# Optimization experiments

Measured on AMD Instinct MI355X. Metric: run time of the kernel, lower is better.

## Reference

```python
import jax, jax.numpy as jnp
import numpy as np

N, CF, CC, H, W, S = 16, 768, 64, 56, 56, 40  # S = feature_samples
EPS = 1e-10


def _norm(t):
    # F.normalize(t, dim=1, eps=1e-10): divide by channel L2 norm clamped to eps
    n = jnp.sqrt(jnp.sum(t * t, axis=1, keepdims=True))
    return t / jnp.maximum(n, EPS)


def _grid_sample(t, grid):
    """Bilinear grid_sample, padding_mode='border', align_corners=True.
    t: [N,C,H,W]; grid: [N,Ho,Wo,2] with (x,y) in [-1,1]. Returns [N,C,Ho,Wo]."""
    Ht, Wt = t.shape[2], t.shape[3]
    x = (grid[..., 0] + 1.0) * 0.5 * (Wt - 1)
    y = (grid[..., 1] + 1.0) * 0.5 * (Ht - 1)
    # border padding == clamp sampling coords to valid range
    x = jnp.clip(x, 0.0, Wt - 1)
    y = jnp.clip(y, 0.0, Ht - 1)
    x0 = jnp.floor(x)
    y0 = jnp.floor(y)
    wx = (x - x0)[:, None]  # [N,1,Ho,Wo]
    wy = (y - y0)[:, None]
    x0i = x0.astype(jnp.int32)
    y0i = y0.astype(jnp.int32)
    x1i = jnp.minimum(x0i + 1, Wt - 1)
    y1i = jnp.minimum(y0i + 1, Ht - 1)

    def gather(img, yi, xi):  # img [C,H,W], yi/xi [Ho,Wo] -> [C,Ho,Wo]
        return img[:, yi, xi]

    g = jax.vmap(gather)
    v00 = g(t, y0i, x0i)
    v01 = g(t, y0i, x1i)
    v10 = g(t, y1i, x0i)
    v11 = g(t, y1i, x1i)
    return (v00 * (1 - wx) * (1 - wy) + v01 * wx * (1 - wy)
            + v10 * (1 - wx) * wy + v11 * wx * wy)


def _corr(a, b):
    return jnp.einsum('nchw,ncij->nhwij', a, b)


def setup_inputs() -> dict:
    key = jax.random.key(0)
    k = jax.random.split(key, 6)
    return {
        'orig_feats': jax.random.normal(k[0], (N, CF, H, W), jnp.float32),
        'orig_feats_pos': jax.random.normal(k[1], (N, CF, H, W), jnp.float32),
        'orig_code': jax.random.normal(k[2], (N, CC, H, W), jnp.float32),
        'orig_code_pos': jax.random.normal(k[3], (N, CC, H, W), jnp.float32),
        'coords1': jax.random.uniform(k[4], (N, S, S, 2), jnp.float32),
        'coords2': jax.random.uniform(k[5], (N, S, S, 2), jnp.float32),
    }


def reference(orig_feats, orig_feats_pos, orig_code, orig_code_pos, coords1, coords2):
    # torch.rand(...)*2 - 1, then sample() permutes grid dims (0,2,1,3)
    g1 = jnp.transpose(coords1 * 2.0 - 1.0, (0, 2, 1, 3))
    g2 = jnp.transpose(coords2 * 2.0 - 1.0, (0, 2, 1, 3))
    feats = _grid_sample(orig_feats, g1)
    code = _grid_sample(orig_code, g1)
    feats_pos = _grid_sample(orig_feats_pos, g2)
    code_pos = _grid_sample(orig_code_pos, g2)

    fd = _corr(_norm(feats), _norm(feats_pos))           # [N,S,S,S,S]
    old_mean = jnp.mean(fd)
    fd = fd - jnp.mean(fd, axis=(3, 4), keepdims=True)
    fd = fd - jnp.mean(fd) + old_mean
    cd = _corr(_norm(code), _norm(code_pos))             # [N,S,S,S,S]
    loss = jnp.mean(-jnp.maximum(cd, 0.0) * fd)
    return loss
```

## Files before the change

### kernel.cpp

```cpp
#include <hip/hip_runtime.h>
#include <hip/hip_bf16.h>

#define NN 16
#define CF 768
#define CC 64
#define HH 56
#define WW 56
#define SS 40
#define PP (SS*SS)
#define PPAD 1664
#define NPT (NN*PP)
#define NPTP (NN*PPAD)
#define HWP (HH*WW)

typedef __attribute__((ext_vector_type(8))) short short8;
typedef __attribute__((ext_vector_type(4))) float f32x4;

typedef const __attribute__((address_space(1))) void* gas_p;
typedef __attribute__((address_space(3))) void* las_p;

__device__ __forceinline__ unsigned f2b(float f) {
    __hip_bfloat16 b = __float2bfloat16(f);
    return (unsigned)*(unsigned short*)&b;
}
__device__ __forceinline__ float bup(unsigned u, int hi) {
    unsigned bits = hi ? (u & 0xffff0000u) : (u << 16);
    return __uint_as_float(bits);
}

__device__ __forceinline__ void bilin(float gx, float gy,
    int& o00, int& o01, int& o10, int& o11,
    float& w00, float& w01, float& w10, float& w11)
{
    float x = (gx + 1.f) * 0.5f * (float)(WW - 1);
    float y = (gy + 1.f) * 0.5f * (float)(HH - 1);
    x = fminf(fmaxf(x, 0.f), (float)(WW - 1));
    y = fminf(fmaxf(y, 0.f), (float)(HH - 1));
    float xf = floorf(x), yf = floorf(y);
    int x0 = (int)xf, y0 = (int)yf;
    int x1 = min(x0 + 1, WW - 1), y1 = min(y0 + 1, HH - 1);
    float wx = x - xf, wy = y - yf;
    w00 = (1.f-wx)*(1.f-wy); w01 = wx*(1.f-wy); w10 = (1.f-wx)*wy; w11 = wx*wy;
    o00 = y0*WW + x0; o01 = y0*WW + x1; o10 = y1*WW + x0; o11 = y1*WW + x1;
}

__global__ __launch_bounds__(256) void k_sample(
    const float* __restrict__ f0, const float* __restrict__ f1,
    const float* __restrict__ c0in, const float* __restrict__ c1in,
    const float* __restrict__ g0, const float* __restrict__ g1,
    float* __restrict__ nrmF, float* __restrict__ nrmC,
    unsigned char* __restrict__ OF0, unsigned char* __restrict__ OF1,
    short* __restrict__ OC0, short* __restrict__ OC1)
{
    const int flat = blockIdx.x;
    const int q    = (flat >> 3) & 3;
    const int u    = ((flat >> 5) << 3) | (flat & 7);
    const int set  = u / 416;
    const int rem  = u % 416;
    const int n    = rem / 26;
    const int v    = rem % 26;
    const bool isF = v < 24;
    const int ks   = isF ? v : v - 24;
    const int g    = ks * 4 + q;

    const float* src0; float* nrm;
    if (isF) {
        src0 = (set ? f1 : f0) + ((size_t)n * CF + g * 8) * HWP;
        nrm  = nrmF + (size_t)set * NPTP;
    } else {
        src0 = (set ? c1in : c0in) + ((size_t)n * CC + g * 8) * HWP;
        nrm  = nrmC + (size_t)set * NPTP;
    }
    unsigned char* outF = set ? OF1 : OF0;
    short*         outC = set ? OC1 : OC0;
    const float* gr = set ? g1 : g0;
    const int t = threadIdx.x;

    __shared__ float plane[2][4096];

    int   po[7], pdx[7], pdw[7];
    float pw[7][4];
    #pragma unroll
    for (int i = 0; i < 7; i++) {
        int p = t + i * 256;
        if (p < PP) {
            float2 gg = *(const float2*)&gr[2 * (n * PP + p)];
            int o00, o01, o10, o11; float w00, w01, w10, w11;
            bilin(gg.x*2.f - 1.f, gg.y*2.f - 1.f, o00, o01, o10, o11, w00, w01, w10, w11);
            po[i] = o00; pdx[i] = o01 - o00; pdw[i] = o10 - o00;
            pw[i][0] = w00; pw[i][1] = w01; pw[i][2] = w10; pw[i][3] = w11;
        } else {
            po[i] = 0; pdx[i] = 0; pdw[i] = 0;
            pw[i][0] = pw[i][1] = pw[i][2] = pw[i][3] = 0.f;
        }
    }

    auto* pl3 = (__attribute__((address_space(3))) char*)&plane[0][0];

#define ISSUE(C)                                                                    \
    do {                                                                            \
        const char* sp_ = (const char*)(src0 + (C) * HWP);                          \
        _Pragma("unroll")                                                           \
        for (int i_ = 0; i_ < 4; i_++) {                                            \
            int j_  = t + i_ * 256;                                                 \
            int jc_ = min(j_, 783);                                                 \
            __builtin_amdgcn_global_load_lds((gas_p)(sp_ + jc_ * 16),               \
                (las_p)(pl3 + (((C) & 1) * 16384 + j_ * 16)), 16, 0, 0);            \
        }                                                                           \
    } while (0)

    float ss[7];
    float fv[7][8];
    #pragma unroll
    for (int i = 0; i < 7; i++) ss[i] = 0.f;

    ISSUE(0);
    #pragma unroll
    for (int c = 0; c < 8; c++) {
        if (c < 7) {
            ISSUE(c + 1);
            asm volatile("s_waitcnt vmcnt(4)" ::: "memory");
        } else {
            asm volatile("s_waitcnt vmcnt(0)" ::: "memory");
        }
        __builtin_amdgcn_sched_barrier(0);
        __builtin_amdgcn_s_barrier();
        const float* pl = &plane[c & 1][0];
        #pragma unroll
        for (int i = 0; i < 7; i++) {
            float val = pw[i][0] * pl[po[i]]
                      + pw[i][1] * pl[po[i] + pdx[i]]
                      + pw[i][2] * pl[po[i] + pdw[i]]
                      + pw[i][3] * pl[po[i] + pdw[i] + pdx[i]];
            ss[i] += val * val;
            fv[i][c] = val;
        }
        __builtin_amdgcn_sched_barrier(0);
        __builtin_amdgcn_s_barrier();
    }
#undef ISSUE

    if (isF) {
        const size_t ob = ((size_t)((n * 24 + ks) * 4 + q)) * PPAD * 8;
        #pragma unroll
        for (int i = 0; i < 7; i++) {
            int p = t + i * 256;
            if (p < PPAD) {
                unsigned w0 = 0u, w1 = 0u;
                w0 = __builtin_amdgcn_cvt_pk_fp8_f32(fv[i][0], fv[i][1], w0, 0);
                w0 = __builtin_amdgcn_cvt_pk_fp8_f32(fv[i][2], fv[i][3], w0, 1);
                w1 = __builtin_amdgcn_cvt_pk_fp8_f32(fv[i][4], fv[i][5], w1, 0);
                w1 = __builtin_amdgcn_cvt_pk_fp8_f32(fv[i][6], fv[i][7], w1, 1);
                uint2 w; w.x = w0; w.y = w1;
                *(uint2*)&outF[ob + (size_t)p * 8] = w;
                if (p < PP) atomicAdd(&nrm[n * PPAD + p], ss[i]);
            }
        }
    } else {
        const size_t ob = ((size_t)(n * 2 + ks)) * PPAD * 32 + q * 8;
        #pragma unroll
        for (int i = 0; i < 7; i++) {
            int p = t + i * 256;
            if (p < PPAD) {
                short ov[8] __attribute__((aligned(16)));
                #pragma unroll
                for (int c = 0; c < 8; c++) {
                    __hip_bfloat16 b = __float2bfloat16(fv[i][c]);
                    ov[c] = *(short*)&b;
                }
                *(short8*)&outC[ob + (size_t)p * 32] = *(const short8*)ov;
                if (p < PP) atomicAdd(&nrm[n * PPAD + p], ss[i]);
            }
        }
    }
}

__global__ __launch_bounds__(256) void k_nrm(
    const float* __restrict__ nrmF, const float* __restrict__ nrmC,
    float* __restrict__ sclF, float* __restrict__ sclC)
{
    const int i = blockIdx.x * 256 + threadIdx.x;
    if (i >= 2 * NPTP) return;
    const float* nrm = blockIdx.y ? nrmC : nrmF;
    float*       scl = blockIdx.y ? sclC : sclF;
    const int p = i % PPAD;
    float s = (p < PP) ? 1.f / fmaxf(sqrtf(nrm[i]), 1e-10f) : 0.f;
    scl[i] = s;
}

__global__ __launch_bounds__(256, 3) void k_corr(
    const unsigned char* __restrict__ A, const unsigned char* __restrict__ B,
    const short* __restrict__ C, const short* __restrict__ D,
    const float* __restrict__ sF, const float* __restrict__ sC,
    float* __restrict__ rowfd, float* __restrict__ rowrc, float* __restrict__ t1out)
{
    const int flat = blockIdx.x;
    const int v   = (flat & 7) * 338 + (flat >> 3);
    const int n   = v / 169;
    const int rr  = v - n * 169;
    const int bp1 = (rr / 13) * 128;
    const int bp2 = (rr % 13) * 128;

    __shared__ char Asb[3][8192];
    __shared__ char Bsb[3][8192];

    const int t    = threadIdx.x;
    const int wv   = t >> 6, lane = t & 63;
    const int wm   = wv >> 1, wn = wv & 1;
    const int frow = lane & 15, fcg = lane >> 4;
    const int fslot = fcg ^ ((frow >> 1) & 3);

    const int sg0  = wv * 2 * 64 + lane;
    const int row0 = sg0 >> 2,        cg0 = (sg0 & 3) ^ ((row0 >> 1) & 3);
    const int sg1  = sg0 + 64;
    const int row1 = sg1 >> 2,        cg1 = (sg1 & 3) ^ ((row1 >> 1) & 3);
    const size_t kstep_s = (size_t)PPAD * 32;
    const short* cdC = C + (size_t)n * 2 * kstep_s;
    const short* cdD = D + (size_t)n * 2 * kstep_s;
    const size_t toA0 = (size_t)(bp1 + row0) * 32 + cg0 * 8;
    const size_t toA1 = (size_t)(bp1 + row1) * 32 + cg1 * 8;
    const size_t toB0 = (size_t)(bp2 + row0) * 32 + cg0 * 8;
    const size_t toB1 = (size_t)(bp2 + row1) * 32 + cg1 * 8;
    auto* As3s = (__attribute__((address_space(3))) short*)&Asb[0][0];
    auto* Bs3s = (__attribute__((address_space(3))) short*)&Bsb[0][0];
    const short* AsS = (const short*)&Asb[0][0];
    const short* BsS = (const short*)&Bsb[0][0];
    const int ldsA0 = (wv * 2    ) * 512;
    const int ldsA1 = (wv * 2 + 1) * 512;

    const size_t FDTILE = (size_t)PPAD * 64;
    const unsigned char* fdA = A + (size_t)n * 24 * ((size_t)PPAD * 32);
    const unsigned char* fdB = B + (size_t)n * 24 * ((size_t)PPAD * 32);
    const size_t toAf0 = (size_t)(wv * 2    ) * (PPAD * 8) + (size_t)(bp1 + 2 * lane) * 8;
    const size_t toAf1 = (size_t)(wv * 2 + 1) * (PPAD * 8) + (size_t)(bp1 + 2 * lane) * 8;
    const size_t toBf0 = (size_t)(wv * 2    ) * (PPAD * 8) + (size_t)(bp2 + 2 * lane) * 8;
    const size_t toBf1 = (size_t)(wv * 2 + 1) * (PPAD * 8) + (size_t)(bp2 + 2 * lane) * 8;
    auto* Asb3 = (__attribute__((address_space(3))) char*)&Asb[0][0];
    auto* Bsb3 = (__attribute__((address_space(3))) char*)&Bsb[0][0];
    const int fldsW0 = (wv * 2    ) * 1024;
    const int fldsW1 = (wv * 2 + 1) * 1024;

#define STAGECD(BUF, OFF)                                                           \
    do {                                                                            \
        const size_t off_ = (OFF);                                                  \
        const int b_ = (BUF) * 4096;                                                \
        __builtin_amdgcn_global_load_lds((gas_p)(cdC + toA0 + off_),                \
                                         (las_p)(As3s + b_ + ldsA0), 16, 0, 0);     \
        __builtin_amdgcn_global_load_lds((gas_p)(cdC + toA1 + off_),                \
                                         (las_p)(As3s + b_ + ldsA1), 16, 0, 0);     \
        __builtin_amdgcn_global_load_lds((gas_p)(cdD + toB0 + off_),                \
                                         (las_p)(Bs3s + b_ + ldsA0), 16, 0, 0);     \
        __builtin_amdgcn_global_load_lds((gas_p)(cdD + toB1 + off_),                \
                                         (las_p)(Bs3s + b_ + ldsA1), 16, 0, 0);     \
    } while (0)

#define STAGEF(TILE, BUF)                                                           \
    do {                                                                            \
        const size_t off_ = (size_t)(TILE) * FDTILE;                                \
        __builtin_amdgcn_global_load_lds((gas_p)(fdA + toAf0 + off_),               \
                                         (las_p)(Asb3 + (BUF) * 8192 + fldsW0), 16, 0, 0); \
        __builtin_amdgcn_global_load_lds((gas_p)(fdA + toAf1 + off_),               \
                                         (las_p)(Asb3 + (BUF) * 8192 + fldsW1), 16, 0, 0); \
        __builtin_amdgcn_global_load_lds((gas_p)(fdB + toBf0 + off_),               \
                                         (las_p)(Bsb3 + (BUF) * 8192 + fldsW0), 16, 0, 0); \
        __builtin_amdgcn_global_load_lds((gas_p)(fdB + toBf1 + off_),               \
                                         (las_p)(Bsb3 + (BUF) * 8192 + fldsW1), 16, 0, 0); \
    } while (0)

#define COMPUTECD(BUF, ACC)                                                         \
    do {                                                                            \
        short8 af[4], bf[4];                                                        \
        _Pragma("unroll")                                                           \
        for (int m = 0; m < 4; m++)                                                 \
            af[m] = *(const short8*)&AsS[(BUF)*4096 + (wm*64 + m*16 + frow)*32 + fslot*8]; \
        _Pragma("unroll")                                                           \
        for (int q = 0; q < 4; q++)                                                 \
            bf[q] = *(const short8*)&BsS[(BUF)*4096 + (wn*64 + q*16 + frow)*32 + fslot*8]; \
        _Pragma("unroll")                                                           \
        for (int m = 0; m < 4; m++)                                                 \
            _Pragma("unroll")                                                       \
            for (int q = 0; q < 4; q++)                                             \
                ACC[m][q] = __builtin_amdgcn_mfma_f32_16x16x32_bf16(af[m], bf[q], ACC[m][q], 0, 0, 0); \
    } while (0)

#define COMPUTEF64(BUF, ACC)                                                        \
    do {                                                                            \
        _Pragma("unroll")                                                           \
        for (int kk_ = 0; kk_ < 2; kk_++) {                                         \
            long af[4], bf[4];                                                      \
            const int kb_ = (BUF) * 8192 + (kk_ * 4 + fcg) * 1024;                  \
            _Pragma("unroll")                                                       \
            for (int m = 0; m < 4; m++)                                             \
                af[m] = *(const long*)&Asb[0][kb_ + (wm*64 + m*16 + frow)*8];       \
            _Pragma("unroll")                                                       \
            for (int q = 0; q < 4; q++)                                             \
                bf[q] = *(const long*)&Bsb[0][kb_ + (wn*64 + q*16 + frow)*8];       \
            _Pragma("unroll")                                                       \
            for (int m = 0; m < 4; m++)                                             \
                _Pragma("unroll")                                                   \
                for (int q = 0; q < 4; q++)                                         \
                    ACC[m][q] = __builtin_amdgcn_mfma_f32_16x16x32_fp8_fp8(af[m], bf[q], ACC[m][q], 0, 0, 0); \
        }                                                                           \
    } while (0)

#define WAITV4  do { asm volatile("s_waitcnt vmcnt(4)" ::: "memory");               \
                     __builtin_amdgcn_sched_barrier(0);                             \
                     __builtin_amdgcn_s_barrier(); } while (0)
#define WAITV0  do { asm volatile("s_waitcnt vmcnt(0)" ::: "memory");               \
                     __builtin_amdgcn_sched_barrier(0);                             \
                     __builtin_amdgcn_s_barrier(); } while (0)

    unsigned pcd[4][4][2];

    STAGECD(0, 0);
    STAGECD(1, kstep_s);

    {
        f32x4 acccd[4][4];
        #pragma unroll
        for (int m = 0; m < 4; m++)
            #pragma unroll
            for (int q = 0; q < 4; q++)
                #pragma unroll
                for (int r = 0; r < 4; r++) acccd[m][q][r] = 0.f;

        WAITV4;
        STAGEF(0, 2);
        COMPUTECD(0, acccd);
        WAITV4;
        STAGEF(1, 0);
        COMPUTECD(1, acccd);

        #pragma unroll
        for (int m = 0; m < 4; m++)
            #pragma unroll
            for (int q = 0; q < 4; q++) {
                float r0 = fmaxf(acccd[m][q][0], 0.f);
                float r1 = fmaxf(acccd[m][q][1], 0.f);
                float r2 = fmaxf(acccd[m][q][2], 0.f);
                float r3 = fmaxf(acccd[m][q][3], 0.f);
                pcd[m][q][0] = f2b(r0) | (f2b(r1) << 16);
                pcd[m][q][1] = f2b(r2) | (f2b(r3) << 16);
            }
    }

    f32x4 accfd[4][4];
    #pragma unroll
    for (int m = 0; m < 4; m++)
        #pragma unroll
        for (int q = 0; q < 4; q++)
            #pragma unroll
            for (int r = 0; r < 4; r++) accfd[m][q][r] = 0.f;

    for (int kp = 0; kp < 4; kp++) {
        const int tb = 3 * kp;
        WAITV4;
        STAGEF(tb + 2, 1);
        COMPUTEF64(2, accfd);
        WAITV4;
        if (kp < 3) STAGEF(tb + 3, 2);
        COMPUTEF64(0, accfd);
        if (kp < 3) {
            WAITV4;
            STAGEF(tb + 4, 0);
        } else {
            WAITV0;
        }
        COMPUTEF64(1, accfd);
    }
#undef STAGECD
#undef STAGEF
#undef COMPUTECD
#undef COMPUTEF64
#undef WAITV4
#undef WAITV0

    float scc_[4], sfc_[4];
    #pragma unroll
    for (int q = 0; q < 4; q++) {
        size_t colp = (size_t)NPTP + (size_t)n * PPAD + bp2 + wn*64 + q*16 + frow;
        scc_[q] = sC[colp];
        sfc_[q] = sF[colp];
    }

    float t1 = 0.f;
    #pragma unroll
    for (int m = 0; m < 4; m++) {
        #pragma unroll
        for (int r = 0; r < 4; r++) {
            size_t rowp = (size_t)n * PPAD + bp1 + wm*64 + m*16 + fcg*4 + r;
            float scr = sC[rowp];
            float sfr = sF[rowp];
            float sf = 0.f, sr = 0.f;
            #pragma unroll
            for (int q = 0; q < 4; q++) {
                float fdv = accfd[m][q][r] * sfr * sfc_[q];
                float rcv = bup(pcd[m][q][r >> 1], r & 1) * scr * scc_[q];
                t1 += rcv * fdv;
                sf += fdv;
                sr += rcv;
            }
            #pragma unroll
            for (int d = 1; d < 16; d <<= 1) {
                sf += __shfl_xor(sf, d, 64);
                sr += __shfl_xor(sr, d, 64);
            }
            if ((lane & 15) == 0) {
                int row = bp1 + wm*64 + m*16 + fcg*4 + r;
                atomicAdd(&rowfd[n * PPAD + row], sf);
                atomicAdd(&rowrc[n * PPAD + row], sr);
            }
        }
    }
    #pragma unroll
    for (int d = 1; d < 64; d <<= 1) t1 += __shfl_xor(t1, d, 64);
    __shared__ float t1s[4];
    if (lane == 0) t1s[wv] = t1;
    __syncthreads();
    if (t == 0) atomicAdd(t1out, t1s[0] + t1s[1] + t1s[2] + t1s[3]);
}

__global__ __launch_bounds__(1024) void k_final(
    const float* __restrict__ rowfd, const float* __restrict__ rowrc,
    const float* __restrict__ t1p, float* __restrict__ out)
{
    const int t = threadIdx.x;
    double cr = 0.0, sf = 0.0, sr = 0.0;
    for (int i = t; i < NN * PPAD; i += 1024) {
        double a = rowfd[i], b = rowrc[i];
        cr += a * b; sf += a; sr += b;
    }
    __shared__ double sh[1024];
    sh[t] = cr; __syncthreads();
    for (int s = 512; s > 0; s >>= 1) { if (t < s) sh[t] += sh[t + s]; __syncthreads(); }
    cr = sh[0]; __syncthreads();
    sh[t] = sf; __syncthreads();
    for (int s = 512; s > 0; s >>= 1) { if (t < s) sh[t] += sh[t + s]; __syncthreads(); }
    sf = sh[0]; __syncthreads();
    sh[t] = sr; __syncthreads();
    for (int s = 512; s > 0; s >>= 1) { if (t < s) sh[t] += sh[t + s]; __syncthreads(); }
    sr = sh[0];
    if (t == 0) {
        double M = (double)NN * (double)PP * (double)PP;
        double t1 = (double)t1p[0];
        double bracket = t1 - cr / (double)PP + (sf / M) * sr;
        out[0] = (float)(-bracket / M);
    }
}

extern "C" void kernel_launch(void* const* d_in, const int* in_sizes, int n_in,
                              void* d_out, int out_size, void* d_ws, size_t ws_size,
                              hipStream_t stream)
{
    const float* orig_feats     = (const float*)d_in[0];
    const float* orig_feats_pos = (const float*)d_in[1];
    const float* orig_code      = (const float*)d_in[2];
    const float* orig_code_pos  = (const float*)d_in[3];
    const float* coords1        = (const float*)d_in[4];
    const float* coords2        = (const float*)d_in[5];

    char* ws = (char*)d_ws;
    float* t1    = (float*)(ws + 0);
    float* rowfd = (float*)(ws + 256);
    float* rowrc = (float*)(ws + 106752);
    float* nrmF  = (float*)(ws + 213248);
    float* nrmC  = (float*)(ws + 426240);
    const size_t zeroBytes = 639232;
    float* sclF  = (float*)(ws + 639232);
    float* sclC  = (float*)(ws + 852224);
    unsigned char* OF0 = (unsigned char*)(ws + 1065216);
    unsigned char* OF1 = (unsigned char*)(ws + 1065216 + 20447232ull);
    short* OC0 = (short*)(ws + 1065216 + 2*20447232ull);
    short* OC1 = (short*)(ws + 1065216 + 2*20447232ull + 3407872ull);

    (void)hipMemsetAsync(d_ws, 0, zeroBytes, stream);

    k_sample<<<dim3(3328), 256, 0, stream>>>(
        orig_feats, orig_feats_pos, orig_code, orig_code_pos,
        coords1, coords2, nrmF, nrmC, OF0, OF1, OC0, OC1);

    k_nrm<<<dim3((2*NPTP + 255)/256, 2), 256, 0, stream>>>(
        nrmF, nrmC, sclF, sclC);

    k_corr<<<dim3(2704), 256, 0, stream>>>(
        OF0, OF1, OC0, OC1, sclF, sclC, rowfd, rowrc, t1);

    k_final<<<1, 1024, 0, stream>>>(rowfd, rowrc, t1, (float*)d_out);
}
```

Measured before the change: 211.5 us.

## Widen correlation tile to 128x256 with 512 threads and compute code correlation at epilogue

The correlation kernel now uses 512-thread blocks with 8 waves, each block covering a 128x256 output tile. This halves the block count and raises reuse of the A-side feature data. The code-correlation MFMAs move from a prologue, where results were packed to bf16 to save registers, to an epilogue that recomputes them per row group from data staged after the feature loop. That removes the bf16 rounding of the code correlation and frees registers held across the main loop. The cost is a larger LDS footprint, clamped padded columns in the last tile column that do wasted work, and an extra serial staging phase before the epilogue.

```diff
diff --git a/kernel.cpp b/kernel.cpp
--- a/kernel.cpp
+++ b/kernel.cpp
@@ -18,15 +18,6 @@
 
 typedef const __attribute__((address_space(1))) void* gas_p;
 typedef __attribute__((address_space(3))) void* las_p;
-
-__device__ __forceinline__ unsigned f2b(float f) {
-    __hip_bfloat16 b = __float2bfloat16(f);
-    return (unsigned)*(unsigned short*)&b;
-}
-__device__ __forceinline__ float bup(unsigned u, int hi) {
-    unsigned bits = hi ? (u & 0xffff0000u) : (u << 16);
-    return __uint_as_float(bits);
-}
 
 __device__ __forceinline__ void bilin(float gx, float gy,
     int& o00, int& o01, int& o10, int& o11,
@@ -188,110 +179,93 @@
     scl[i] = s;
 }
 
-__global__ __launch_bounds__(256, 3) void k_corr(
+__global__ __launch_bounds__(512, 4) void k_corr(
     const unsigned char* __restrict__ A, const unsigned char* __restrict__ B,
     const short* __restrict__ C, const short* __restrict__ D,
     const float* __restrict__ sF, const float* __restrict__ sC,
     float* __restrict__ rowfd, float* __restrict__ rowrc, float* __restrict__ t1out)
 {
     const int flat = blockIdx.x;
-    const int v   = (flat & 7) * 338 + (flat >> 3);
-    const int n   = v / 169;
-    const int rr  = v - n * 169;
-    const int bp1 = (rr / 13) * 128;
-    const int bp2 = (rr % 13) * 128;
+    const int v   = (flat & 7) * 182 + (flat >> 3);
+    const int n   = v / 91;
+    const int rr  = v - n * 91;
+    const int bp1 = (rr / 7) * 128;
+    const int bp2 = (rr % 7) * 256;
 
     __shared__ char Asb[3][8192];
-    __shared__ char Bsb[3][8192];
+    __shared__ char Bsb[3][16384];
+    __shared__ float t1s[8];
 
     const int t    = threadIdx.x;
     const int wv   = t >> 6, lane = t & 63;
-    const int wm   = wv >> 1, wn = wv & 1;
+    const int wm   = wv >> 2, wn = wv & 3;
     const int frow = lane & 15, fcg = lane >> 4;
     const int fslot = fcg ^ ((frow >> 1) & 3);
-
-    const int sg0  = wv * 2 * 64 + lane;
-    const int row0 = sg0 >> 2,        cg0 = (sg0 & 3) ^ ((row0 >> 1) & 3);
-    const int sg1  = sg0 + 64;
-    const int row1 = sg1 >> 2,        cg1 = (sg1 & 3) ^ ((row1 >> 1) & 3);
-    const size_t kstep_s = (size_t)PPAD * 32;
-    const short* cdC = C + (size_t)n * 2 * kstep_s;
-    const short* cdD = D + (size_t)n * 2 * kstep_s;
-    const size_t toA0 = (size_t)(bp1 + row0) * 32 + cg0 * 8;
-    const size_t toA1 = (size_t)(bp1 + row1) * 32 + cg1 * 8;
-    const size_t toB0 = (size_t)(bp2 + row0) * 32 + cg0 * 8;
-    const size_t toB1 = (size_t)(bp2 + row1) * 32 + cg1 * 8;
-    auto* As3s = (__attribute__((address_space(3))) short*)&Asb[0][0];
-    auto* Bs3s = (__attribute__((address_space(3))) short*)&Bsb[0][0];
-    const short* AsS = (const short*)&Asb[0][0];
-    const short* BsS = (const short*)&Bsb[0][0];
-    const int ldsA0 = (wv * 2    ) * 512;
-    const int ldsA1 = (wv * 2 + 1) * 512;
 
     const size_t FDTILE = (size_t)PPAD * 64;
     const unsigned char* fdA = A + (size_t)n * 24 * ((size_t)PPAD * 32);
     const unsigned char* fdB = B + (size_t)n * 24 * ((size_t)PPAD * 32);
-    const size_t toAf0 = (size_t)(wv * 2    ) * (PPAD * 8) + (size_t)(bp1 + 2 * lane) * 8;
-    const size_t toAf1 = (size_t)(wv * 2 + 1) * (PPAD * 8) + (size_t)(bp1 + 2 * lane) * 8;
-    const size_t toBf0 = (size_t)(wv * 2    ) * (PPAD * 8) + (size_t)(bp2 + 2 * lane) * 8;
-    const size_t toBf1 = (size_t)(wv * 2 + 1) * (PPAD * 8) + (size_t)(bp2 + 2 * lane) * 8;
+    const size_t toAf  = (size_t)wv * (PPAD * 8) + (size_t)(bp1 + 2 * lane) * 8;
+    const int rB0 = min(bp2 +       2 * lane, PPAD - 2);
+    const int rB1 = min(bp2 + 128 + 2 * lane, PPAD - 2);
+    const size_t toBf0 = (size_t)wv * (PPAD * 8) + (size_t)rB0 * 8;
+    const size_t toBf1 = (size_t)wv * (PPAD * 8) + (size_t)rB1 * 8;
     auto* Asb3 = (__attribute__((address_space(3))) char*)&Asb[0][0];
     auto* Bsb3 = (__attribute__((address_space(3))) char*)&Bsb[0][0];
-    const int fldsW0 = (wv * 2    ) * 1024;
-    const int fldsW1 = (wv * 2 + 1) * 1024;
-
-#define STAGECD(BUF, OFF)                                                           \
-    do {                                                                            \
-        const size_t off_ = (OFF);                                                  \
-        const int b_ = (BUF) * 4096;                                                \
-        __builtin_amdgcn_global_load_lds((gas_p)(cdC + toA0 + off_),                \
-                                         (las_p)(As3s + b_ + ldsA0), 16, 0, 0);     \
-        __builtin_amdgcn_global_load_lds((gas_p)(cdC + toA1 + off_),                \
-                                         (las_p)(As3s + b_ + ldsA1), 16, 0, 0);     \
-        __builtin_amdgcn_global_load_lds((gas_p)(cdD + toB0 + off_),                \
-                                         (las_p)(Bs3s + b_ + ldsA0), 16, 0, 0);     \
-        __builtin_amdgcn_global_load_lds((gas_p)(cdD + toB1 + off_),                \
-                                         (las_p)(Bs3s + b_ + ldsA1), 16, 0, 0);     \
-    } while (0)
+    const int ldsA  = wv * 1024;
+    const int ldsB0 = wv * 2048;
+    const int ldsB1 = wv * 2048 + 1024;
+
+    const short* cdC = C + (size_t)n * 2 * ((size_t)PPAD * 32);
+    const short* cdD = D + (size_t)n * 2 * ((size_t)PPAD * 32);
+    const int gA   = wv * 64 + lane;
+    const int rowA = gA >> 2;
+    const int cgA  = (gA & 3) ^ ((rowA >> 1) & 3);
+    const size_t toAc = (size_t)(bp1 + rowA) * 32 + cgA * 8;
+    const int gB0  = wv * 128 + lane, gB1 = gB0 + 64;
+    const int rowB0 = gB0 >> 2, rowB1 = gB1 >> 2;
+    const int cgB0 = (gB0 & 3) ^ ((rowB0 >> 1) & 3);
+    const int cgB1 = (gB1 & 3) ^ ((rowB1 >> 1) & 3);
+    const size_t toBc0 = (size_t)min(bp2 + rowB0, PPAD - 1) * 32 + cgB0 * 8;
+    const size_t toBc1 = (size_t)min(bp2 + rowB1, PPAD - 1) * 32 + cgB1 * 8;
+    auto* As3s = (__attribute__((address_space(3))) short*)&Asb[0][0];
+    auto* Bs3s = (__attribute__((address_space(3))) short*)&Bsb[0][0];
+    const int ldsAc  = wv * 512;
+    const int ldsBc0 = wv * 1024;
+    const int ldsBc1 = wv * 1024 + 512;
 
 #define STAGEF(TILE, BUF)                                                           \
     do {                                                                            \
         const size_t off_ = (size_t)(TILE) * FDTILE;                                \
-        __builtin_amdgcn_global_load_lds((gas_p)(fdA + toAf0 + off_),               \
-                                         (las_p)(Asb3 + (BUF) * 8192 + fldsW0), 16, 0, 0); \
-        __builtin_amdgcn_global_load_lds((gas_p)(fdA + toAf1 + off_),               \
-                                         (las_p)(Asb3 + (BUF) * 8192 + fldsW1), 16, 0, 0); \
+        __builtin_amdgcn_global_load_lds((gas_p)(fdA + toAf + off_),                \
+            (las_p)(Asb3 + (BUF) * 8192 + ldsA), 16, 0, 0);                         \
         __builtin_amdgcn_global_load_lds((gas_p)(fdB + toBf0 + off_),               \
-                                         (las_p)(Bsb3 + (BUF) * 8192 + fldsW0), 16, 0, 0); \
+            (las_p)(Bsb3 + (BUF) * 16384 + ldsB0), 16, 0, 0);                       \
         __builtin_amdgcn_global_load_lds((gas_p)(fdB + toBf1 + off_),               \
-                                         (las_p)(Bsb3 + (BUF) * 8192 + fldsW1), 16, 0, 0); \
+            (las_p)(Bsb3 + (BUF) * 16384 + ldsB1), 16, 0, 0);                       \
     } while (0)
 
-#define COMPUTECD(BUF, ACC)                                                         \
+#define STAGECD(KS)                                                                 \
     do {                                                                            \
-        short8 af[4], bf[4];                                                        \
-        _Pragma("unroll")                                                           \
-        for (int m = 0; m < 4; m++)                                                 \
-            af[m] = *(const short8*)&AsS[(BUF)*4096 + (wm*64 + m*16 + frow)*32 + fslot*8]; \
-        _Pragma("unroll")                                                           \
-        for (int q = 0; q < 4; q++)                                                 \
-            bf[q] = *(const short8*)&BsS[(BUF)*4096 + (wn*64 + q*16 + frow)*32 + fslot*8]; \
-        _Pragma("unroll")                                                           \
-        for (int m = 0; m < 4; m++)                                                 \
-            _Pragma("unroll")                                                       \
-            for (int q = 0; q < 4; q++)                                             \
-                ACC[m][q] = __builtin_amdgcn_mfma_f32_16x16x32_bf16(af[m], bf[q], ACC[m][q], 0, 0, 0); \
+        const size_t o_ = (size_t)(KS) * ((size_t)PPAD * 32);                       \
+        __builtin_amdgcn_global_load_lds((gas_p)(cdC + toAc + o_),                  \
+            (las_p)(As3s + (KS) * 4096 + ldsAc), 16, 0, 0);                         \
+        __builtin_amdgcn_global_load_lds((gas_p)(cdD + toBc0 + o_),                 \
+            (las_p)(Bs3s + (KS) * 8192 + ldsBc0), 16, 0, 0);                        \
+        __builtin_amdgcn_global_load_lds((gas_p)(cdD + toBc1 + o_),                 \
+            (las_p)(Bs3s + (KS) * 8192 + ldsBc1), 16, 0, 0);                        \
     } while (0)
 
 #define COMPUTEF64(BUF, ACC)                                                        \
     do {                                                                            \
         _Pragma("unroll")                                                           \
         for (int kk_ = 0; kk_ < 2; kk_++) {                                         \
+            const int ka_ = (BUF) * 8192  + (kk_ * 4 + fcg) * 1024;                 \
+            const int kb_ = (BUF) * 16384 + (kk_ * 4 + fcg) * 2048;                 \
             long af[4], bf[4];                                                      \
-            const int kb_ = (BUF) * 8192 + (kk_ * 4 + fcg) * 1024;                  \
             _Pragma("unroll")                                                       \
             for (int m = 0; m < 4; m++)                                             \
-                af[m] = *(const long*)&Asb[0][kb_ + (wm*64 + m*16 + frow)*8];       \
+                af[m] = *(const long*)&Asb[0][ka_ + (wm*64 + m*16 + frow)*8];       \
             _Pragma("unroll")                                                       \
             for (int q = 0; q < 4; q++)                                             \
                 bf[q] = *(const long*)&Bsb[0][kb_ + (wn*64 + q*16 + frow)*8];       \
@@ -303,47 +277,13 @@
         }                                                                           \
     } while (0)
 
-#define WAITV4  do { asm volatile("s_waitcnt vmcnt(4)" ::: "memory");               \
+#define WAITV3  do { asm volatile("s_waitcnt vmcnt(3)" ::: "memory");               \
                      __builtin_amdgcn_sched_barrier(0);                             \
                      __builtin_amdgcn_s_barrier(); } while (0)
 #define WAITV0  do { asm volatile("s_waitcnt vmcnt(0)" ::: "memory");               \
                      __builtin_amdgcn_sched_barrier(0);                             \
                      __builtin_amdgcn_s_barrier(); } while (0)
 
-    unsigned pcd[4][4][2];
-
-    STAGECD(0, 0);
-    STAGECD(1, kstep_s);
-
-    {
-        f32x4 acccd[4][4];
-        #pragma unroll
-        for (int m = 0; m < 4; m++)
-            #pragma unroll
-            for (int q = 0; q < 4; q++)
-                #pragma unroll
-                for (int r = 0; r < 4; r++) acccd[m][q][r] = 0.f;
-
-        WAITV4;
-        STAGEF(0, 2);
-        COMPUTECD(0, acccd);
-        WAITV4;
-        STAGEF(1, 0);
-        COMPUTECD(1, acccd);
-
-        #pragma unroll
-        for (int m = 0; m < 4; m++)
-            #pragma unroll
-            for (int q = 0; q < 4; q++) {
-                float r0 = fmaxf(acccd[m][q][0], 0.f);
-                float r1 = fmaxf(acccd[m][q][1], 0.f);
-                float r2 = fmaxf(acccd[m][q][2], 0.f);
-                float r3 = fmaxf(acccd[m][q][3], 0.f);
-                pcd[m][q][0] = f2b(r0) | (f2b(r1) << 16);
-                pcd[m][q][1] = f2b(r2) | (f2b(r3) << 16);
-            }
-    }
-
     f32x4 accfd[4][4];
     #pragma unroll
     for (int m = 0; m < 4; m++)
@@ -352,33 +292,45 @@
             #pragma unroll
             for (int r = 0; r < 4; r++) accfd[m][q][r] = 0.f;
 
+    STAGEF(0, 0);
+    STAGEF(1, 1);
+
     for (int kp = 0; kp < 4; kp++) {
         const int tb = 3 * kp;
-        WAITV4;
-        STAGEF(tb + 2, 1);
-        COMPUTEF64(2, accfd);
-        WAITV4;
-        if (kp < 3) STAGEF(tb + 3, 2);
+        WAITV3;
+        STAGEF(tb + 2, 2);
         COMPUTEF64(0, accfd);
+        WAITV3;
+        if (kp < 3) STAGEF(tb + 3, 0);
+        COMPUTEF64(1, accfd);
         if (kp < 3) {
-            WAITV4;
-            STAGEF(tb + 4, 0);
+            WAITV3;
+            STAGEF(tb + 4, 1);
         } else {
             WAITV0;
         }
-        COMPUTEF64(1, accfd);
-    }
+        COMPUTEF64(2, accfd);
+    }
+
+    STAGECD(0);
+    STAGECD(1);
+    asm volatile("s_waitcnt vmcnt(0)" ::: "memory");
+    __builtin_amdgcn_sched_barrier(0);
+    __builtin_amdgcn_s_barrier();
+#undef STAGEF
 #undef STAGECD
-#undef STAGEF
-#undef COMPUTECD
 #undef COMPUTEF64
-#undef WAITV4
+#undef WAITV3
 #undef WAITV0
 
+    const short* AsS = (const short*)&Asb[0][0];
+    const short* BsS = (const short*)&Bsb[0][0];
+
     float scc_[4], sfc_[4];
     #pragma unroll
     for (int q = 0; q < 4; q++) {
-        size_t colp = (size_t)NPTP + (size_t)n * PPAD + bp2 + wn*64 + q*16 + frow;
+        int c = min(bp2 + wn*64 + q*16 + frow, PPAD - 1);
+        size_t colp = (size_t)NPTP + (size_t)n * PPAD + c;
         scc_[q] = sC[colp];
         sfc_[q] = sF[colp];
     }
@@ -386,6 +338,20 @@
     float t1 = 0.f;
     #pragma unroll
     for (int m = 0; m < 4; m++) {
+        f32x4 a2[4];
+        #pragma unroll
+        for (int q = 0; q < 4; q++)
+            #pragma unroll
+            for (int r = 0; r < 4; r++) a2[q][r] = 0.f;
+        short8 ac0 = *(const short8*)&AsS[0*4096 + (wm*64 + m*16 + frow)*32 + fslot*8];
+        short8 ac1 = *(const short8*)&AsS[1*4096 + (wm*64 + m*16 + frow)*32 + fslot*8];
+        #pragma unroll
+        for (int q = 0; q < 4; q++) {
+            short8 bc0 = *(const short8*)&BsS[0*8192 + (wn*64 + q*16 + frow)*32 + fslot*8];
+            short8 bc1 = *(const short8*)&BsS[1*8192 + (wn*64 + q*16 + frow)*32 + fslot*8];
+            a2[q] = __builtin_amdgcn_mfma_f32_16x16x32_bf16(ac0, bc0, a2[q], 0, 0, 0);
+            a2[q] = __builtin_amdgcn_mfma_f32_16x16x32_bf16(ac1, bc1, a2[q], 0, 0, 0);
+        }
         #pragma unroll
         for (int r = 0; r < 4; r++) {
             size_t rowp = (size_t)n * PPAD + bp1 + wm*64 + m*16 + fcg*4 + r;
@@ -395,7 +361,7 @@
             #pragma unroll
             for (int q = 0; q < 4; q++) {
                 float fdv = accfd[m][q][r] * sfr * sfc_[q];
-                float rcv = bup(pcd[m][q][r >> 1], r & 1) * scr * scc_[q];
+                float rcv = fmaxf(a2[q][r], 0.f) * scr * scc_[q];
                 t1 += rcv * fdv;
                 sf += fdv;
                 sr += rcv;
@@ -414,10 +380,14 @@
     }
     #pragma unroll
     for (int d = 1; d < 64; d <<= 1) t1 += __shfl_xor(t1, d, 64);
-    __shared__ float t1s[4];
     if (lane == 0) t1s[wv] = t1;
     __syncthreads();
-    if (t == 0) atomicAdd(t1out, t1s[0] + t1s[1] + t1s[2] + t1s[3]);
+    if (t == 0) {
+        float s = 0.f;
+        #pragma unroll
+        for (int w = 0; w < 8; w++) s += t1s[w];
+        atomicAdd(t1out, s);
+    }
 }
 
 __global__ __launch_bounds__(1024) void k_final(
@@ -469,9 +439,9 @@
     float* sclF  = (float*)(ws + 639232);
     float* sclC  = (float*)(ws + 852224);
     unsigned char* OF0 = (unsigned char*)(ws + 1065216);
-    unsigned char* OF1 = (unsigned char*)(ws + 1065216 + 20447232ull);
-    short* OC0 = (short*)(ws + 1065216 + 2*20447232ull);
-    short* OC1 = (short*)(ws + 1065216 + 2*20447232ull + 3407872ull);
+    unsigned char* OF1 = OF0 + 20447232ull;
+    short* OC0 = (short*)(OF1 + 20447232ull);
+    short* OC1 = (short*)((char*)OC0 + 3407872ull);
 
     (void)hipMemsetAsync(d_ws, 0, zeroBytes, stream);
 
@@ -482,7 +452,7 @@
     k_nrm<<<dim3((2*NPTP + 255)/256, 2), 256, 0, stream>>>(
         nrmF, nrmC, sclF, sclC);
 
-    k_corr<<<dim3(2704), 256, 0, stream>>>(
+    k_corr<<<dim3(1456), 512, 0, stream>>>(
         OF0, OF1, OC0, OC1, sclF, sclC, rowfd, rowrc, t1);
 
     k_final<<<1, 1024, 0, stream>>>(rowfd, rowrc, t1, (float*)d_out);
```

Result: slower. 269.0 us (+27.2%).
